# Kernel tuning notes

Measured on AMD Instinct MI355X. Metric: run time of the kernel, lower is better.

## Reference

```python
import jax, jax.numpy as jnp
import numpy as np

WIDTH = 1024
NH = 16
HD = 64
MBS = 16
B = 4
L = 2048
BASE_LR = 1.0
EPS = 1e-6


def gelu_tanh(x):
    return jax.nn.gelu(x, approximate=True)


def gelu_bwd(x):
    t = jnp.tanh(0.79788456 * x * (1 + 0.044715 * x * x))
    return 0.5 * x * ((1 - t * t) * (0.79788456 + 0.1070322243 * x * x)) + 0.5 * (1 + t)


def ln_fwd(x, g, b):
    mu = x.mean(-1, keepdims=True)
    var = ((x - mu) ** 2).mean(-1, keepdims=True)
    return g * ((x - mu) * jax.lax.rsqrt(var + EPS)) + b


def ln_l2_bwd(x, tgt, g, b):
    # grad of 0.5*||LN(x)-tgt||^2 wrt x
    mu = x.mean(-1, keepdims=True)
    var = ((x - mu) ** 2).mean(-1, keepdims=True)
    std = jnp.sqrt(var + EPS)
    xh = (x - mu) / std
    gx = (g * xh + b - tgt) * g
    return (gx - gx.mean(-1, keepdims=True) - xh * (gx * xh).mean(-1, keepdims=True)) / std


def adapter_forward(hidden_states, Wq, Wk, Wv, Wo, Wg, lr_w, lr_b,
                    learnable_token_idx, norm_w, norm_b, W1, b1, W2, b2,
                    post_w, post_b):
    Bb, Ll, width = hidden_states.shape
    nh, hd = norm_w.shape
    mbs = learnable_token_idx.shape[0]
    nc = Ll // mbs  # L chosen divisible by mini_batch_size

    def split_heads(x):  # [B,L,width] -> [B,nh,nc,mbs,hd]
        return x.reshape(Bb, Ll, nh, hd).transpose(0, 2, 1, 3).reshape(Bb, nh, nc, mbs, hd)

    XQ = split_heads(hidden_states @ Wq.T)
    XK = split_heads(hidden_states @ Wk.T)
    XV = split_heads(hidden_states @ Wv.T)

    # eta: learnable per-token lr gate (get_eta)
    X = hidden_states.reshape(Bb, nc, mbs, width)
    lr = jnp.einsum('bnkc,hdc->bhnkd', X, lr_w) + lr_b.reshape(1, nh, 1, 1, 1)
    lr = jax.nn.sigmoid(lr).transpose(0, 1, 2, 4, 3)  # [B,nh,nc,1,mbs]
    lr_eta = BASE_LR * lr / hd
    token_idx = jnp.clip(1.0 / jnp.arange(1, mbs + 1, dtype=hidden_states.dtype)
                         + learnable_token_idx, 0.0, None)
    token_eta = token_idx.reshape(1, 1, 1, mbs, 1)
    eta = token_eta * lr_eta  # [B,nh,nc,mbs,mbs]

    tril = jnp.tril(jnp.ones((mbs, mbs), dtype=hidden_states.dtype))
    lnw = norm_w.reshape(nh, 1, hd)
    lnb = norm_b.reshape(nh, 1, hd)

    def step(carry, xs):
        W1s, b1s, W2s, b2s = carry  # [B,nh,hd,4hd], [B,nh,1,4hd], [B,nh,4hd,hd], [B,nh,1,hd]
        XQm, XKm, XVm, etam = xs    # [B,nh,mbs,hd] x3, [B,nh,mbs,mbs]
        X1 = XKm
        Z1 = X1 @ W1s + b1s
        X2 = gelu_tanh(Z1)
        Z2 = X2 @ W2s + b2s
        gZ2 = ln_l2_bwd(Z2, XVm - XKm, lnw, lnb)
        gZ1 = (gZ2 @ jnp.swapaxes(W2s, -1, -2)) * gelu_bwd(Z1)
        eta_tril = etam * tril
        Attn1 = tril * (XQm @ jnp.swapaxes(X1, -1, -2))
        b1_bar = b1s - eta_tril @ gZ1
        Z1_bar = XQm @ W1s - (etam * Attn1) @ gZ1 + b1_bar
        X2_bar = gelu_tanh(Z1_bar)
        Attn2 = tril * (X2_bar @ jnp.swapaxes(X2, -1, -2))
        b2_bar = b2s - eta_tril @ gZ2
        Z2_bar = X2_bar @ W2s - (etam * Attn2) @ gZ2 + b2_bar
        last = etam[:, :, -1, :, None]  # [B,nh,mbs,1]
        W1n = W1s - jnp.swapaxes(last * X1, -1, -2) @ gZ1
        b1n = b1s - (last * gZ1).sum(-2, keepdims=True)
        W2n = W2s - jnp.swapaxes(last * X2, -1, -2) @ gZ2
        b2n = b2s - (last * gZ2).sum(-2, keepdims=True)
        XQW = XQm + ln_fwd(Z2_bar, lnw, lnb)
        return (W1n, b1n, W2n, b2n), XQW

    carry0 = (jnp.broadcast_to(W1, (Bb,) + W1.shape),
              jnp.broadcast_to(b1, (Bb,) + b1.shape),
              jnp.broadcast_to(W2, (Bb,) + W2.shape),
              jnp.broadcast_to(b2, (Bb,) + b2.shape))
    xs = tuple(jnp.moveaxis(t, 2, 0) for t in (XQ, XK, XV, eta))
    _, XQW = jax.lax.scan(step, carry0, xs)  # [nc,B,nh,mbs,hd]
    out = XQW.transpose(1, 0, 3, 2, 4).reshape(Bb, Ll, width)

    # post_norm (LayerNorm eps=1e-6)
    out = ln_fwd(out, post_w, post_b)
    # gate
    out = gelu_tanh(hidden_states @ Wg.T) * out
    # o_proj
    return out @ Wo.T


def setup_inputs():
    key = jax.random.key(0)
    ks = jax.random.split(key, 10)
    n = lambda k, s: jax.random.normal(k, s, dtype=jnp.float32) * 0.02
    return {
        'hidden_states': jax.random.normal(ks[0], (B, L, WIDTH), dtype=jnp.float32),
        'Wq': n(ks[1], (WIDTH, WIDTH)),
        'Wk': n(ks[2], (WIDTH, WIDTH)),
        'Wv': n(ks[3], (WIDTH, WIDTH)),
        'Wo': n(ks[4], (WIDTH, WIDTH)),
        'Wg': n(ks[5], (WIDTH, WIDTH)),
        'lr_w': n(ks[6], (NH, 1, WIDTH)),
        'lr_b': jnp.zeros((NH, 1), jnp.float32),
        'learnable_token_idx': jnp.zeros((MBS,), jnp.float32),
        'norm_w': jnp.ones((NH, HD), jnp.float32),
        'norm_b': jnp.zeros((NH, HD), jnp.float32),
        'W1': n(ks[7], (NH, HD, 4 * HD)),
        'b1': jnp.zeros((NH, 1, 4 * HD), jnp.float32),
        'W2': n(ks[8], (NH, 4 * HD, HD)),
        'b2': jnp.zeros((NH, 1, HD), jnp.float32),
        'post_w': jnp.ones((WIDTH,), jnp.float32),
        'post_b': jnp.zeros((WIDTH,), jnp.float32),
    }


def reference(hidden_states, Wq, Wk, Wv, Wo, Wg, lr_w, lr_b, learnable_token_idx,
              norm_w, norm_b, W1, b1, W2, b2, post_w, post_b):
    return adapter_forward(hidden_states, Wq, Wk, Wv, Wo, Wg, lr_w, lr_b,
                           learnable_token_idx, norm_w, norm_b, W1, b1, W2, b2,
                           post_w, post_b)
```

## Files before the change

kernel.cpp:

```cpp
#include <hip/hip_runtime.h>

#define WIDTH 1024
#define MBSZ 16
#define LLL 2048
#define NCHUNK 128

typedef __attribute__((ext_vector_type(4))) float f32x4;
typedef __attribute__((ext_vector_type(2))) float f32x2;
typedef __attribute__((ext_vector_type(8))) short short8;
typedef __attribute__((ext_vector_type(4))) short short4v;
typedef __attribute__((ext_vector_type(2))) unsigned u32x2;
typedef __attribute__((ext_vector_type(4))) unsigned u32x4;

#define MFMA16(a, b, c) __builtin_amdgcn_mfma_f32_16x16x32_bf16((a), (b), (c), 0, 0, 0)

__device__ __forceinline__ short f2bf(float f) {
  unsigned u = __float_as_uint(f);
  u = (u + 0x7FFFu + ((u >> 16) & 1u)) >> 16;
  return (short)u;
}
__device__ __forceinline__ float bf2f(short s) {
  return __uint_as_float(((unsigned)(unsigned short)s) << 16);
}
__device__ __forceinline__ unsigned cvt_pk(float lo, float hi) {
  unsigned r;
  asm("v_cvt_pk_bf16_f32 %0, %1, %2" : "=v"(r) : "v"(lo), "v"(hi));
  return r;
}
__device__ __forceinline__ float fast_e2u(float x) {
  return __builtin_amdgcn_exp2f(x * (2.30220776f + 0.10294322f * x * x));
}
__device__ __forceinline__ float gelu_f(float x) {
  float e = fast_e2u(x);
  return x * (1.0f - __builtin_amdgcn_rcpf(e + 1.0f));
}
__device__ __forceinline__ float gelu_bwd_f(float x) {
  float e = fast_e2u(x);
  float r = __builtin_amdgcn_rcpf(e + 1.0f);
  return 2.0f * x * r * (1.0f - r) * (0.79788456f + 0.1070322243f * x * x) + (1.0f - r);
}
__device__ __forceinline__ int w2row(int d) { return d * 264 + (d >> 3) * 24; }

template <int OUTBF>
__device__ __forceinline__ void gemm_64x128(const short* __restrict__ A,
                                            const short* __restrict__ W,
                                            float* __restrict__ C,
                                            short* __restrict__ Cb,
                                            int m0, int n0,
                                            short* sA, short* sB, int t2) {
  const int wv = t2 >> 6, ln = t2 & 63;
  const int fr = ln & 15, kh = (ln >> 4) * 8;
  const int arow = t2 >> 2, aseg = (t2 & 3) * 8;
  f32x4 acc[8];
#pragma unroll
  for (int s = 0; s < 8; ++s) acc[s] = (f32x4){0.f, 0.f, 0.f, 0.f};
  const short* ga = A + (long)(m0 + arow) * 1024 + aseg;
  const short* gw0 = W + (long)(n0 + arow) * 1024 + aseg;
  const short* gw1 = W + (long)(n0 + 64 + arow) * 1024 + aseg;
  for (int k0 = 0; k0 < 1024; k0 += 32) {
    const short8 a8 = *(const short8*)(ga + k0);
    const short8 w80 = *(const short8*)(gw0 + k0);
    const short8 w81 = *(const short8*)(gw1 + k0);
    *(short8*)&sA[arow * 40 + aseg] = a8;
    *(short8*)&sB[arow * 40 + aseg] = w80;
    *(short8*)&sB[(arow + 64) * 40 + aseg] = w81;
    __syncthreads();
    const short8 af = *(const short8*)&sA[(wv * 16 + fr) * 40 + kh];
#pragma unroll
    for (int s = 0; s < 8; ++s) {
      const short8 bf8 = *(const short8*)&sB[(s * 16 + fr) * 40 + kh];
      acc[s] = MFMA16(af, bf8, acc[s]);
    }
    __syncthreads();
  }
  const int orow = m0 + wv * 16 + (ln >> 4) * 4;
#pragma unroll
  for (int s = 0; s < 8; ++s)
#pragma unroll
    for (int q = 0; q < 4; ++q) {
      const long off = (long)(orow + q) * 1024 + n0 + s * 16 + fr;
      if (OUTBF) Cb[off] = f2bf(acc[s][q]);
      else C[off] = acc[s][q];
    }
}

__global__ __launch_bounds__(256) void cvt_kernel(const float* __restrict__ hs,
                                                  const float* __restrict__ Wq,
                                                  const float* __restrict__ Wk,
                                                  const float* __restrict__ Wv,
                                                  const float* __restrict__ Wg,
                                                  const float* __restrict__ Wo,
                                                  short* __restrict__ dst) {
  const long idx = ((long)blockIdx.x * 256 + threadIdx.x) * 8;
  if (idx >= 13631488L) return;
  const float* src;
  long off;
  if (idx < 8388608L)       { src = hs; off = idx; }
  else if (idx < 9437184L)  { src = Wq; off = idx - 8388608L; }
  else if (idx < 10485760L) { src = Wk; off = idx - 9437184L; }
  else if (idx < 11534336L) { src = Wv; off = idx - 10485760L; }
  else if (idx < 12582912L) { src = Wg; off = idx - 11534336L; }
  else                      { src = Wo; off = idx - 12582912L; }
  const f32x4 a = *(const f32x4*)(src + off);
  const f32x4 b = *(const f32x4*)(src + off + 4);
  u32x4 o;
  o[0] = cvt_pk(a[0], a[1]); o[1] = cvt_pk(a[2], a[3]);
  o[2] = cvt_pk(b[0], b[1]); o[3] = cvt_pk(b[2], b[3]);
  *(u32x4*)(dst + idx) = o;
}

__global__ __launch_bounds__(256) void gemm_final(const short* __restrict__ A,
                                                  const short* __restrict__ W,
                                                  float* __restrict__ C) {
  __shared__ __align__(16) short sA[2560];
  __shared__ __align__(16) short sB[5120];
  gemm_64x128<0>(A, W, C, nullptr, blockIdx.x * 64, blockIdx.y * 128, sA, sB, threadIdx.x);
}

__global__ __launch_bounds__(256) void qkv_lr_kernel(const short* __restrict__ hsb,
                                                     const short* __restrict__ Wqb,
                                                     const short* __restrict__ Wkb,
                                                     const short* __restrict__ Wvb,
                                                     float* __restrict__ Qb,
                                                     float* __restrict__ Kb,
                                                     float* __restrict__ Vb,
                                                     const float* __restrict__ hs,
                                                     const float* __restrict__ lrw,
                                                     const float* __restrict__ lrb,
                                                     float* __restrict__ LRb) {
  __shared__ __align__(16) short sA[2560];
  __shared__ __align__(16) short sB[5120];
  __shared__ __align__(16) float row[1024];
  const int tid = threadIdx.x;
  const int idx = blockIdx.x;
  if (idx < 3072) {
    const int which = idx >> 10, t = idx & 1023;
    const short* W = (which == 0) ? Wqb : (which == 1) ? Wkb : Wvb;
    float* C = (which == 0) ? Qb : (which == 1) ? Kb : Vb;
    gemm_64x128<0>(hsb, W, C, nullptr, (t & 127) * 64, (t >> 7) * 128, sA, sB, tid);
  } else {
    const int t = idx - 3072;
    *(f32x4*)&row[tid * 4] = *(const f32x4*)&hs[(long)t * 1024 + tid * 4];
    __syncthreads();
    const int hh = tid >> 4, j = tid & 15;
    const float* wrow = lrw + hh * 1024;
    float s = 0.f;
#pragma unroll 4
    for (int m = 0; m < 16; ++m) {
      const int c = j * 4 + m * 64;
      f32x4 x = *(const f32x4*)&row[c];
      f32x4 w = *(const f32x4*)&wrow[c];
      s += x[0] * w[0] + x[1] * w[1] + x[2] * w[2] + x[3] * w[3];
    }
#pragma unroll
    for (int o = 8; o; o >>= 1) s += __shfl_xor(s, o, 16);
    if (j == 0) {
      const float v = s + lrb[hh];
      const float sg = 1.f / (1.f + expf(-v));
      const int b = t >> 11, tr = t & 2047;
      LRb[((b << 4) + hh) * 2048 + tr] = sg * (1.f / 64.f);
    }
  }
}

__global__ __launch_bounds__(512, 2) void scan_gate_kernel(
    float* __restrict__ Qb, const float* __restrict__ Kb, const float* __restrict__ Vb,
    const float* __restrict__ LRb, const float* __restrict__ lti,
    const float* __restrict__ nw, const float* __restrict__ nb,
    const float* __restrict__ W1in, const float* __restrict__ b1in,
    const float* __restrict__ W2in, const float* __restrict__ b2in,
    const short* __restrict__ hsA, const short* __restrict__ Wgb,
    short* __restrict__ Gout) {
  __shared__ __align__(16) short sW1b[256 * 72];
  __shared__ __align__(16) short sW2dp[64 * 264 + 192];
  __shared__ __align__(16) short la1T[64 * 24];
  __shared__ __align__(16) short la2T[256 * 24];
  __shared__ __align__(16) short sX1b[16 * 72];
  __shared__ __align__(16) short sXQb[16 * 72];
  __shared__ __align__(16) float sXQf[16 * 68];
  __shared__ __align__(16) float sTg[16 * 72];
  __shared__ __align__(16) short sX2b[16 * 264];
  __shared__ __align__(16) short sXbb[16 * 264];
  __shared__ __align__(16) short sG1c[256 * 24];
  __shared__ __align__(16) short sG2b[16 * 72];
  __shared__ __align__(16) short sG2c[64 * 24];
  __shared__ __align__(16) float sZ2f[16 * 68];
  __shared__ __align__(16) short sC1b[16 * 24];
  __shared__ __align__(16) short sC2b[16 * 24];
  __shared__ __align__(16) float sB1[256];
  __shared__ __align__(16) float sB2[64];
  __shared__ float sLr[16];
  __shared__ float sTok[16];
  __shared__ __align__(16) float sLnw[64];
  __shared__ __align__(16) float sLnb[64];

  const int tid = threadIdx.x;

  if (blockIdx.x >= 64) {
    const int hh = tid >> 8, t2 = tid & 255;
    const int tile = (blockIdx.x - 64) * 2 + hh;
    short* sAh = sW1b + hh * 7680;
    short* sBh = sAh + 2560;
    gemm_64x128<1>(hsA, Wgb, nullptr, Gout, (tile & 127) * 64, (tile >> 7) * 128, sAh, sBh, t2);
    return;
  }

  const int bh = blockIdx.x, b = bh >> 4, h = bh & 15;
  const int w = tid >> 6, ln = tid & 63;
  const int fr = ln & 15, half = ln >> 4, hk = half * 8;
  const int nt0 = 2 * w;

  float w1m[8][4], w2m[8][4];
#pragma unroll
  for (int r = 0; r < 8; ++r) {
    const int T = w * 8 + r, dt = T >> 4, pt = T & 15;
#pragma unroll
    for (int qq = 0; qq < 4; ++qq) {
      w1m[r][qq] = W1in[h * 16384 + (dt * 16 + half * 4 + qq) * 256 + pt * 16 + fr];
      w2m[r][qq] = W2in[h * 16384 + (pt * 16 + half * 4 + qq) * 64 + dt * 16 + fr];
    }
  }
  for (int e = tid; e < 16384; e += 512) {
    {
      const int d = e >> 8, p = e & 255;
      sW1b[p * 72 + d] = f2bf(W1in[h * 16384 + e]);
    }
    {
      const int p = e >> 6, d = e & 63;
      sW2dp[w2row(d) + (p ^ (((d >> 3) & 3) << 3))] = f2bf(W2in[h * 16384 + e]);
    }
  }
  if (tid < 256) sB1[tid] = b1in[h * 256 + tid];
  if (tid < 64) { sB2[tid] = b2in[h * 64 + tid]; sLnw[tid] = nw[h * 64 + tid]; sLnb[tid] = nb[h * 64 + tid]; }
  if (tid < 16) sTok[tid] = fmaxf(1.0f / (float)(tid + 1) + lti[tid], 0.0f);

  const f32x4 zf4 = (f32x4){0.f, 0.f, 0.f, 0.f};
  short8 zs8;
#pragma unroll
  for (int j = 0; j < 8; ++j) zs8[j] = 0;

  const int pf_i = tid >> 5;
  const int pf_d = (tid & 31) * 2;
  f32x2 pk, pq, pv;
  float plr = 0.f;
  {
    const long a0 = ((long)(b * LLL + pf_i)) * WIDTH + h * 64 + pf_d;
    pk = *(const f32x2*)&Kb[a0];
    pq = *(const f32x2*)&Qb[a0];
    pv = *(const f32x2*)&Vb[a0];
    if (tid < 16) plr = LRb[(long)bh * 2048 + tid];
  }

  for (int n = 0; n < NCHUNK; ++n) {
    const long gbase = ((long)(b * LLL + n * MBSZ)) * WIDTH + h * 64;

    {
      *(unsigned*)&sX1b[pf_i * 72 + pf_d] = cvt_pk(pk[0], pk[1]);
      *(unsigned*)&sXQb[pf_i * 72 + pf_d] = cvt_pk(pq[0], pq[1]);
      sXQf[pf_i * 68 + pf_d] = pq[0];
      sXQf[pf_i * 68 + pf_d + 1] = pq[1];
      sTg[pf_i * 72 + pf_d] = pv[0] - pk[0];
      sTg[pf_i * 72 + pf_d + 1] = pv[1] - pk[1];
      if (tid < 16) sLr[tid] = plr;
    }
    __syncthreads();

    short8 aX1[2], aXQ[2];
    aX1[0] = *(const short8*)&sX1b[fr * 72 + hk];
    aX1[1] = *(const short8*)&sX1b[fr * 72 + 32 + hk];
    aXQ[0] = *(const short8*)&sXQb[fr * 72 + hk];
    aXQ[1] = *(const short8*)&sXQb[fr * 72 + 32 + hk];
    f32x4 z1[2], q1[2];
    float b1p[2];
#pragma unroll
    for (int t = 0; t < 2; ++t) {
      const int p = (nt0 + t) * 16 + fr;
      z1[t] = zf4; q1[t] = zf4;
#pragma unroll
      for (int ks = 0; ks < 2; ++ks) {
        short8 bw = *(const short8*)&sW1b[p * 72 + ks * 32 + hk];
        z1[t] = MFMA16(aX1[ks], bw, z1[t]);
        q1[t] = MFMA16(aXQ[ks], bw, q1[t]);
      }
      b1p[t] = sB1[p];
#pragma unroll
      for (int qq = 0; qq < 4; ++qq) {
        z1[t][qq] += b1p[t];
        sX2b[(half * 4 + qq) * 264 + p] = f2bf(gelu_f(z1[t][qq]));
      }
    }
    {
      const float tok15 = sTok[15];
      const int d = tid >> 3, j0 = (tid & 7) * 2;
      const float v0 = bf2f(sX1b[j0 * 72 + d]) * (tok15 * sLr[j0]);
      const float v1 = bf2f(sX1b[(j0 + 1) * 72 + d]) * (tok15 * sLr[j0 + 1]);
      *(unsigned*)&la1T[d * 24 + j0] = cvt_pk(v0, v1);
    }
    if (w == 0) {
      f32x4 c = MFMA16(aXQ[0], aX1[0], zf4);
      c = MFMA16(aXQ[1], aX1[1], c);
#pragma unroll
      for (int qq = 0; qq < 4; ++qq) {
        const int i = half * 4 + qq, j = fr;
        sC1b[i * 24 + j] = f2bf((i >= j) ? sTok[i] * sLr[j] * (c[qq] + 1.0f) : 0.0f);
      }
    }
    __syncthreads();

    float bb2old = 0.f;
    if (w < 4) {
      const int d = w * 16 + fr;
      const int sw = ((d >> 3) & 3) << 3;
      const int rb = w2row(d);
      f32x4 za = zf4, zb = zf4;
#pragma unroll
      for (int ks = 0; ks < 4; ++ks) {
        short8 a = *(const short8*)&sX2b[fr * 264 + ks * 32 + hk];
        short8 bfr = *(const short8*)&sW2dp[rb + ((ks * 32 + hk) ^ sw)];
        za = MFMA16(a, bfr, za);
      }
#pragma unroll
      for (int ks = 4; ks < 8; ++ks) {
        short8 a = *(const short8*)&sX2b[fr * 264 + ks * 32 + hk];
        short8 bfr = *(const short8*)&sW2dp[rb + ((ks * 32 + hk) ^ sw)];
        zb = MFMA16(a, bfr, zb);
      }
      bb2old = sB2[d];
#pragma unroll
      for (int qq = 0; qq < 4; ++qq)
        sZ2f[(half * 4 + qq) * 68 + d] = za[qq] + zb[qq] + bb2old;
    }
    __syncthreads();

    if (tid < 256) {
      const int i = tid >> 4, j4 = tid & 15;
      const f32x4 z = *(const f32x4*)&sZ2f[i * 68 + j4 * 4];
      float s1 = z[0] + z[1] + z[2] + z[3];
      float s2 = z[0] * z[0] + z[1] * z[1] + z[2] * z[2] + z[3] * z[3];
#pragma unroll
      for (int o = 8; o; o >>= 1) { s1 += __shfl_xor(s1, o, 16); s2 += __shfl_xor(s2, o, 16); }
      const float mu = s1 * (1.f / 64.f);
      const float rstd = rsqrtf(s2 * (1.f / 64.f) - mu * mu + 1e-6f);
      const f32x4 g = *(const f32x4*)&sLnw[j4 * 4];
      const f32x4 bb = *(const f32x4*)&sLnb[j4 * 4];
      const f32x4 tg = *(const f32x4*)&sTg[i * 72 + j4 * 4];
      f32x4 xh, gx;
      float a1 = 0.f, a2 = 0.f;
#pragma unroll
      for (int e = 0; e < 4; ++e) {
        xh[e] = (z[e] - mu) * rstd;
        gx[e] = (g[e] * xh[e] + bb[e] - tg[e]) * g[e];
        a1 += gx[e]; a2 += gx[e] * xh[e];
      }
#pragma unroll
      for (int o = 8; o; o >>= 1) { a1 += __shfl_xor(a1, o, 16); a2 += __shfl_xor(a2, o, 16); }
      const float m1 = a1 * (1.f / 64.f), m2 = a2 * (1.f / 64.f);
      float o4[4];
#pragma unroll
      for (int e = 0; e < 4; ++e) o4[e] = (gx[e] - m1 - xh[e] * m2) * rstd;
      const unsigned lo = cvt_pk(o4[0], o4[1]);
      const unsigned hi = cvt_pk(o4[2], o4[3]);
      *(u32x2*)&sG2b[i * 72 + j4 * 4] = (u32x2){lo, hi};
      sG2c[(j4 * 4 + 0) * 24 + i] = (short)lo;
      sG2c[(j4 * 4 + 1) * 24 + i] = (short)(lo >> 16);
      sG2c[(j4 * 4 + 2) * 24 + i] = (short)hi;
      sG2c[(j4 * 4 + 3) * 24 + i] = (short)(hi >> 16);
    } else {
      const int pp = tid - 256;
      const float tok15 = sTok[15];
      unsigned uu[8];
#pragma unroll
      for (int jp = 0; jp < 8; ++jp) {
        const float v0 = bf2f(sX2b[(2 * jp) * 264 + pp]) * (tok15 * sLr[2 * jp]);
        const float v1 = bf2f(sX2b[(2 * jp + 1) * 264 + pp]) * (tok15 * sLr[2 * jp + 1]);
        uu[jp] = cvt_pk(v0, v1);
      }
      *(u32x4*)&la2T[pp * 24] = (u32x4){uu[0], uu[1], uu[2], uu[3]};
      *(u32x4*)&la2T[pp * 24 + 8] = (u32x4){uu[4], uu[5], uu[6], uu[7]};
    }
    __syncthreads();

    {
      short8 aG2[2];
      aG2[0] = *(const short8*)&sG2b[fr * 72 + hk];
      aG2[1] = *(const short8*)&sG2b[fr * 72 + 32 + hk];
#pragma unroll
      for (int t = 0; t < 2; ++t) {
        const int p = (nt0 + t) * 16 + fr;
        f32x4 g = zf4;
#pragma unroll
        for (int ks = 0; ks < 2; ++ks) {
          const int dg = ks * 32 + hk;
          const int rb2 = w2row(dg) + (p ^ (((dg >> 3) & 3) << 3));
          short8 bw;
#pragma unroll
          for (int jj = 0; jj < 8; ++jj) bw[jj] = sW2dp[rb2 + jj * 264];
          g = MFMA16(aG2[ks], bw, g);
        }
        const unsigned lo = cvt_pk(g[0] * gelu_bwd_f(z1[t][0]), g[1] * gelu_bwd_f(z1[t][1]));
        const unsigned hi = cvt_pk(g[2] * gelu_bwd_f(z1[t][2]), g[3] * gelu_bwd_f(z1[t][3]));
        *(u32x2*)&sG1c[p * 24 + half * 4] = (u32x2){lo, hi};
      }
    }
    if (tid < 64) {
      float s = 0.f;
#pragma unroll
      for (int k = 0; k < 4; ++k) {
        const short4v g4 = *(const short4v*)&sG2c[tid * 24 + k * 4];
        const f32x4 lr4 = *(const f32x4*)&sLr[k * 4];
        s += lr4[0] * bf2f(g4[0]) + lr4[1] * bf2f(g4[1]) +
             lr4[2] * bf2f(g4[2]) + lr4[3] * bf2f(g4[3]);
      }
      sB2[tid] -= sTok[15] * s;
    }
    __syncthreads();

    {
      short8 ac = zs8;
      if (half < 2) ac = *(const short8*)&sC1b[fr * 24 + hk];
#pragma unroll
      for (int t = 0; t < 2; ++t) {
        const int p = (nt0 + t) * 16 + fr;
        short8 bg = zs8;
        if (half < 2) bg = *(const short8*)&sG1c[p * 24 + hk];
        f32x4 corr = MFMA16(ac, bg, zf4);
#pragma unroll
        for (int qq = 0; qq < 4; ++qq)
          sXbb[(half * 4 + qq) * 264 + p] = f2bf(gelu_f(q1[t][qq] + b1p[t] - corr[qq]));
      }
    }
    {
#pragma unroll
      for (int r = 0; r < 8; ++r) {
        const int T = w * 8 + r, dt = T >> 4, pt = T & 15;
        short8 af = zs8, bg = zs8;
        if (half < 2) {
          af = *(const short8*)&la1T[(dt * 16 + fr) * 24 + hk];
          bg = *(const short8*)&sG1c[(pt * 16 + fr) * 24 + hk];
        }
        f32x4 dl = MFMA16(af, bg, zf4);
        const int pp = pt * 16 + fr, d0 = dt * 16 + half * 4;
        w1m[r][0] -= dl[0]; w1m[r][1] -= dl[1]; w1m[r][2] -= dl[2]; w1m[r][3] -= dl[3];
        const unsigned lo = cvt_pk(w1m[r][0], w1m[r][1]);
        const unsigned hi = cvt_pk(w1m[r][2], w1m[r][3]);
        *(u32x2*)&sW1b[pp * 72 + d0] = (u32x2){lo, hi};
      }
    }
    if (tid < 256) {
      float s = 0.f;
#pragma unroll
      for (int k = 0; k < 4; ++k) {
        const short4v g4 = *(const short4v*)&sG1c[tid * 24 + k * 4];
        const f32x4 lr4 = *(const f32x4*)&sLr[k * 4];
        s += lr4[0] * bf2f(g4[0]) + lr4[1] * bf2f(g4[1]) +
             lr4[2] * bf2f(g4[2]) + lr4[3] * bf2f(g4[3]);
      }
      sB1[tid] -= sTok[15] * s;
    }
    __syncthreads();

    {
      const int nn = (n + 1 < NCHUNK) ? n + 1 : n;
      const long a1 = ((long)(b * LLL + nn * MBSZ + pf_i)) * WIDTH + h * 64 + pf_d;
      pk = *(const f32x2*)&Kb[a1];
      pq = *(const f32x2*)&Qb[a1];
      pv = *(const f32x2*)&Vb[a1];
      if (tid < 16) plr = LRb[(long)bh * 2048 + nn * MBSZ + tid];
    }
    f32x4 zbar = zf4;
    if (w < 4) {
      const int d = w * 16 + fr;
      const int sw = ((d >> 3) & 3) << 3;
      const int rb = w2row(d);
      f32x4 za = zf4, zb = zf4;
#pragma unroll
      for (int ks = 0; ks < 4; ++ks) {
        short8 a = *(const short8*)&sXbb[fr * 264 + ks * 32 + hk];
        short8 bfr = *(const short8*)&sW2dp[rb + ((ks * 32 + hk) ^ sw)];
        za = MFMA16(a, bfr, za);
      }
#pragma unroll
      for (int ks = 4; ks < 8; ++ks) {
        short8 a = *(const short8*)&sXbb[fr * 264 + ks * 32 + hk];
        short8 bfr = *(const short8*)&sW2dp[rb + ((ks * 32 + hk) ^ sw)];
        zb = MFMA16(a, bfr, zb);
      }
      zbar[0] = za[0] + zb[0]; zbar[1] = za[1] + zb[1];
      zbar[2] = za[2] + zb[2]; zbar[3] = za[3] + zb[3];
    } else if (w == 4) {
      f32x4 c = zf4;
#pragma unroll
      for (int ks = 0; ks < 8; ++ks) {
        short8 a = *(const short8*)&sXbb[fr * 264 + ks * 32 + hk];
        short8 bx = *(const short8*)&sX2b[fr * 264 + ks * 32 + hk];
        c = MFMA16(a, bx, c);
      }
#pragma unroll
      for (int qq = 0; qq < 4; ++qq) {
        const int i = half * 4 + qq, j = fr;
        sC2b[i * 24 + j] = f2bf((i >= j) ? sTok[i] * sLr[j] * (c[qq] + 1.0f) : 0.0f);
      }
    }
    __syncthreads();

    if (w < 4) {
      const int d = w * 16 + fr;
      short8 ac = zs8, bg = zs8;
      if (half < 2) {
        ac = *(const short8*)&sC2b[fr * 24 + hk];
        bg = *(const short8*)&sG2c[d * 24 + hk];
      }
      f32x4 corr = MFMA16(ac, bg, zf4);
#pragma unroll
      for (int qq = 0; qq < 4; ++qq)
        sZ2f[(half * 4 + qq) * 68 + d] = zbar[qq] + bb2old - corr[qq];
    }
    {
#pragma unroll
      for (int r = 0; r < 8; ++r) {
        const int T = w * 8 + r, pt = T & 15, dt = T >> 4;
        short8 af = zs8, bg = zs8;
        if (half < 2) {
          af = *(const short8*)&la2T[(pt * 16 + fr) * 24 + hk];
          bg = *(const short8*)&sG2c[(dt * 16 + fr) * 24 + hk];
        }
        f32x4 dl = MFMA16(af, bg, zf4);
        const int dd = dt * 16 + fr;
        const int swp = ((dd >> 3) & 3) << 3;
        const int p0 = pt * 16 + half * 4;
        w2m[r][0] -= dl[0]; w2m[r][1] -= dl[1]; w2m[r][2] -= dl[2]; w2m[r][3] -= dl[3];
        const unsigned lo = cvt_pk(w2m[r][0], w2m[r][1]);
        const unsigned hi = cvt_pk(w2m[r][2], w2m[r][3]);
        *(u32x2*)&sW2dp[w2row(dd) + (p0 ^ swp)] = (u32x2){lo, hi};
      }
    }
    __syncthreads();

    if (tid < 256) {
      const int i = tid >> 4, j4 = tid & 15;
      const f32x4 z = *(const f32x4*)&sZ2f[i * 68 + j4 * 4];
      float s1 = z[0] + z[1] + z[2] + z[3];
      float s2 = z[0] * z[0] + z[1] * z[1] + z[2] * z[2] + z[3] * z[3];
#pragma unroll
      for (int o = 8; o; o >>= 1) { s1 += __shfl_xor(s1, o, 16); s2 += __shfl_xor(s2, o, 16); }
      const float mu = s1 * (1.f / 64.f);
      const float rstd = rsqrtf(s2 * (1.f / 64.f) - mu * mu + 1e-6f);
      const f32x4 g = *(const f32x4*)&sLnw[j4 * 4];
      const f32x4 bb = *(const f32x4*)&sLnb[j4 * 4];
      const f32x4 xq = *(const f32x4*)&sXQf[i * 68 + j4 * 4];
      f32x4 o4;
#pragma unroll
      for (int e = 0; e < 4; ++e) o4[e] = xq[e] + g[e] * ((z[e] - mu) * rstd) + bb[e];
      *(f32x4*)&Qb[gbase + (long)i * WIDTH + j4 * 4] = o4;
    }
    __syncthreads();
  }
}

__global__ __launch_bounds__(256) void epi_kernel(const float* __restrict__ X,
                                                  const short* __restrict__ G,
                                                  const float* __restrict__ pw,
                                                  const float* __restrict__ pb,
                                                  short* __restrict__ T) {
  __shared__ float red[8];
  const int t = blockIdx.x, tid = threadIdx.x;
  const long base = (long)t * 1024 + tid * 4;
  f32x4 x = *(const f32x4*)&X[base];
  float s1 = x[0] + x[1] + x[2] + x[3];
  float s2 = x[0] * x[0] + x[1] * x[1] + x[2] * x[2] + x[3] * x[3];
#pragma unroll
  for (int o = 32; o; o >>= 1) { s1 += __shfl_xor(s1, o, 64); s2 += __shfl_xor(s2, o, 64); }
  const int wv = tid >> 6, ln = tid & 63;
  if (ln == 0) { red[wv] = s1; red[4 + wv] = s2; }
  __syncthreads();
  s1 = red[0] + red[1] + red[2] + red[3];
  s2 = red[4] + red[5] + red[6] + red[7];
  const float mu = s1 * (1.f / 1024.f);
  const float rstd = rsqrtf(s2 * (1.f / 1024.f) - mu * mu + 1e-6f);
  const short4v g4 = *(const short4v*)&G[base];
  f32x4 w = *(const f32x4*)&pw[tid * 4];
  f32x4 bb = *(const f32x4*)&pb[tid * 4];
  float o4[4];
#pragma unroll
  for (int e = 0; e < 4; ++e) {
    float y = w[e] * ((x[e] - mu) * rstd) + bb[e];
    o4[e] = gelu_f(bf2f(g4[e])) * y;
  }
  *(u32x2*)&T[base] = (u32x2){cvt_pk(o4[0], o4[1]), cvt_pk(o4[2], o4[3])};
}

extern "C" void kernel_launch(void* const* d_in, const int* in_sizes, int n_in,
                              void* d_out, int out_size, void* d_ws, size_t ws_size,
                              hipStream_t stream) {
  const float* hs  = (const float*)d_in[0];
  const float* Wq  = (const float*)d_in[1];
  const float* Wk  = (const float*)d_in[2];
  const float* Wv  = (const float*)d_in[3];
  const float* Wo  = (const float*)d_in[4];
  const float* Wg  = (const float*)d_in[5];
  const float* lrw = (const float*)d_in[6];
  const float* lrb = (const float*)d_in[7];
  const float* lti = (const float*)d_in[8];
  const float* nw  = (const float*)d_in[9];
  const float* nb  = (const float*)d_in[10];
  const float* W1  = (const float*)d_in[11];
  const float* b1  = (const float*)d_in[12];
  const float* W2  = (const float*)d_in[13];
  const float* b2  = (const float*)d_in[14];
  const float* pw  = (const float*)d_in[15];
  const float* pb  = (const float*)d_in[16];
  float* out = (float*)d_out;
  float* ws = (float*)d_ws;

  float* Qb  = ws;
  float* Kb  = ws + 8388608;
  float* Vb  = ws + 16777216;
  float* LRb = ws + 25165824;
  short* hsb = (short*)(ws + 25296896);
  short* Wqb = hsb + 8388608;
  short* Wkb = Wqb + 1048576;
  short* Wvb = Wkb + 1048576;
  short* Wgb = Wvb + 1048576;
  short* Wob = Wgb + 1048576;
  short* Tb  = (short*)Kb;
  short* Gbb = (short*)out;

  cvt_kernel<<<6656, 256, 0, stream>>>(hs, Wq, Wk, Wv, Wg, Wo, hsb);
  qkv_lr_kernel<<<11264, 256, 0, stream>>>(hsb, Wqb, Wkb, Wvb, Qb, Kb, Vb, hs, lrw, lrb, LRb);
  scan_gate_kernel<<<576, 512, 0, stream>>>(Qb, Kb, Vb, LRb, lti, nw, nb, W1, b1, W2, b2,
                                            hsb, Wgb, Gbb);
  epi_kernel<<<8192, 256, 0, stream>>>(Qb, Gbb, pw, pb, Tb);
  gemm_final<<<dim3(128, 8), 256, 0, stream>>>(Tb, Wob, out);
}
```

Baseline: 918.1 us.

## Double-buffer chunk inputs in LDS and merge barrier phases in scan loop

Chunk inputs (K, Q, V-K target and lr gate) now go into double-buffered shared arrays. Idle threads 256-511 write the next chunk's data during the final LayerNorm/output phase instead of in a separate phase with its own barrier at the top of the loop. The b2 update is moved into the same phase as the corrected-activation computation, which removes another __syncthreads per chunk. Prefetch loads are widened to float4 on half the threads. The cost is more LDS and fewer threads doing the prefetch.

Result: no change. 928.7 us (+1.1%).

```diff
diff --git a/kernel.cpp b/kernel.cpp
--- a/kernel.cpp
+++ b/kernel.cpp
@@ -175,10 +175,10 @@
   __shared__ __align__(16) short sW2dp[64 * 264 + 192];
   __shared__ __align__(16) short la1T[64 * 24];
   __shared__ __align__(16) short la2T[256 * 24];
-  __shared__ __align__(16) short sX1b[16 * 72];
-  __shared__ __align__(16) short sXQb[16 * 72];
-  __shared__ __align__(16) float sXQf[16 * 68];
-  __shared__ __align__(16) float sTg[16 * 72];
+  __shared__ __align__(16) short sX1b[2][16 * 72];
+  __shared__ __align__(16) short sXQb[2][16 * 72];
+  __shared__ __align__(16) float sXQf[2][16 * 68];
+  __shared__ __align__(16) float sTg[2][16 * 72];
   __shared__ __align__(16) short sX2b[16 * 264];
   __shared__ __align__(16) short sXbb[16 * 264];
   __shared__ __align__(16) short sG1c[256 * 24];
@@ -189,7 +189,7 @@
   __shared__ __align__(16) short sC2b[16 * 24];
   __shared__ __align__(16) float sB1[256];
   __shared__ __align__(16) float sB2[64];
-  __shared__ float sLr[16];
+  __shared__ float sLr2[2][16];
   __shared__ float sTok[16];
   __shared__ __align__(16) float sLnw[64];
   __shared__ __align__(16) float sLnb[64];
@@ -239,37 +239,37 @@
 #pragma unroll
   for (int j = 0; j < 8; ++j) zs8[j] = 0;
 
-  const int pf_i = tid >> 5;
-  const int pf_d = (tid & 31) * 2;
-  f32x2 pk, pq, pv;
+  const int ct = tid - 256;
+  const int ci = ct >> 4;
+  const int cd = (ct & 15) * 4;
+  f32x4 pk4, pq4, pv4;
   float plr = 0.f;
-  {
-    const long a0 = ((long)(b * LLL + pf_i)) * WIDTH + h * 64 + pf_d;
-    pk = *(const f32x2*)&Kb[a0];
-    pq = *(const f32x2*)&Qb[a0];
-    pv = *(const f32x2*)&Vb[a0];
-    if (tid < 16) plr = LRb[(long)bh * 2048 + tid];
-  }
+  if (tid >= 256) {
+    const long a0 = ((long)(b * LLL + ci)) * WIDTH + h * 64 + cd;
+    pk4 = *(const f32x4*)&Kb[a0];
+    pq4 = *(const f32x4*)&Qb[a0];
+    pv4 = *(const f32x4*)&Vb[a0];
+    if (ct < 16) plr = LRb[(long)bh * 2048 + ct];
+    *(u32x2*)&sX1b[0][ci * 72 + cd] = (u32x2){cvt_pk(pk4[0], pk4[1]), cvt_pk(pk4[2], pk4[3])};
+    *(u32x2*)&sXQb[0][ci * 72 + cd] = (u32x2){cvt_pk(pq4[0], pq4[1]), cvt_pk(pq4[2], pq4[3])};
+    *(f32x4*)&sXQf[0][ci * 68 + cd] = pq4;
+    f32x4 tg4;
+#pragma unroll
+    for (int e = 0; e < 4; ++e) tg4[e] = pv4[e] - pk4[e];
+    *(f32x4*)&sTg[0][ci * 72 + cd] = tg4;
+    if (ct < 16) sLr2[0][ct] = plr;
+  }
+  __syncthreads();
 
   for (int n = 0; n < NCHUNK; ++n) {
+    const int cb = n & 1;
     const long gbase = ((long)(b * LLL + n * MBSZ)) * WIDTH + h * 64;
 
-    {
-      *(unsigned*)&sX1b[pf_i * 72 + pf_d] = cvt_pk(pk[0], pk[1]);
-      *(unsigned*)&sXQb[pf_i * 72 + pf_d] = cvt_pk(pq[0], pq[1]);
-      sXQf[pf_i * 68 + pf_d] = pq[0];
-      sXQf[pf_i * 68 + pf_d + 1] = pq[1];
-      sTg[pf_i * 72 + pf_d] = pv[0] - pk[0];
-      sTg[pf_i * 72 + pf_d + 1] = pv[1] - pk[1];
-      if (tid < 16) sLr[tid] = plr;
-    }
-    __syncthreads();
-
     short8 aX1[2], aXQ[2];
-    aX1[0] = *(const short8*)&sX1b[fr * 72 + hk];
-    aX1[1] = *(const short8*)&sX1b[fr * 72 + 32 + hk];
-    aXQ[0] = *(const short8*)&sXQb[fr * 72 + hk];
-    aXQ[1] = *(const short8*)&sXQb[fr * 72 + 32 + hk];
+    aX1[0] = *(const short8*)&sX1b[cb][fr * 72 + hk];
+    aX1[1] = *(const short8*)&sX1b[cb][fr * 72 + 32 + hk];
+    aXQ[0] = *(const short8*)&sXQb[cb][fr * 72 + hk];
+    aXQ[1] = *(const short8*)&sXQb[cb][fr * 72 + 32 + hk];
     f32x4 z1[2], q1[2];
     float b1p[2];
 #pragma unroll
@@ -292,8 +292,8 @@
     {
       const float tok15 = sTok[15];
       const int d = tid >> 3, j0 = (tid & 7) * 2;
-      const float v0 = bf2f(sX1b[j0 * 72 + d]) * (tok15 * sLr[j0]);
-      const float v1 = bf2f(sX1b[(j0 + 1) * 72 + d]) * (tok15 * sLr[j0 + 1]);
+      const float v0 = bf2f(sX1b[cb][j0 * 72 + d]) * (tok15 * sLr2[cb][j0]);
+      const float v1 = bf2f(sX1b[cb][(j0 + 1) * 72 + d]) * (tok15 * sLr2[cb][j0 + 1]);
       *(unsigned*)&la1T[d * 24 + j0] = cvt_pk(v0, v1);
     }
     if (w == 0) {
@@ -302,7 +302,7 @@
 #pragma unroll
       for (int qq = 0; qq < 4; ++qq) {
         const int i = half * 4 + qq, j = fr;
-        sC1b[i * 24 + j] = f2bf((i >= j) ? sTok[i] * sLr[j] * (c[qq] + 1.0f) : 0.0f);
+        sC1b[i * 24 + j] = f2bf((i >= j) ? sTok[i] * sLr2[cb][j] * (c[qq] + 1.0f) : 0.0f);
       }
     }
     __syncthreads();
@@ -343,7 +343,7 @@
       const float rstd = rsqrtf(s2 * (1.f / 64.f) - mu * mu + 1e-6f);
       const f32x4 g = *(const f32x4*)&sLnw[j4 * 4];
       const f32x4 bb = *(const f32x4*)&sLnb[j4 * 4];
-      const f32x4 tg = *(const f32x4*)&sTg[i * 72 + j4 * 4];
+      const f32x4 tg = *(const f32x4*)&sTg[cb][i * 72 + j4 * 4];
       f32x4 xh, gx;
       float a1 = 0.f, a2 = 0.f;
 #pragma unroll
@@ -371,8 +371,8 @@
       unsigned uu[8];
 #pragma unroll
       for (int jp = 0; jp < 8; ++jp) {
-        const float v0 = bf2f(sX2b[(2 * jp) * 264 + pp]) * (tok15 * sLr[2 * jp]);
-        const float v1 = bf2f(sX2b[(2 * jp + 1) * 264 + pp]) * (tok15 * sLr[2 * jp + 1]);
+        const float v0 = bf2f(sX2b[(2 * jp) * 264 + pp]) * (tok15 * sLr2[cb][2 * jp]);
+        const float v1 = bf2f(sX2b[(2 * jp + 1) * 264 + pp]) * (tok15 * sLr2[cb][2 * jp + 1]);
         uu[jp] = cvt_pk(v0, v1);
       }
       *(u32x4*)&la2T[pp * 24] = (u32x4){uu[0], uu[1], uu[2], uu[3]};
@@ -402,19 +402,6 @@
         *(u32x2*)&sG1c[p * 24 + half * 4] = (u32x2){lo, hi};
       }
     }
-    if (tid < 64) {
-      float s = 0.f;
-#pragma unroll
-      for (int k = 0; k < 4; ++k) {
-        const short4v g4 = *(const short4v*)&sG2c[tid * 24 + k * 4];
-        const f32x4 lr4 = *(const f32x4*)&sLr[k * 4];
-        s += lr4[0] * bf2f(g4[0]) + lr4[1] * bf2f(g4[1]) +
-             lr4[2] * bf2f(g4[2]) + lr4[3] * bf2f(g4[3]);
-      }
-      sB2[tid] -= sTok[15] * s;
-    }
-    __syncthreads();
-
     {
       short8 ac = zs8;
       if (half < 2) ac = *(const short8*)&sC1b[fr * 24 + hk];
@@ -429,6 +416,19 @@
           sXbb[(half * 4 + qq) * 264 + p] = f2bf(gelu_f(q1[t][qq] + b1p[t] - corr[qq]));
       }
     }
+    if (tid < 64) {
+      float s = 0.f;
+#pragma unroll
+      for (int k = 0; k < 4; ++k) {
+        const short4v g4 = *(const short4v*)&sG2c[tid * 24 + k * 4];
+        const f32x4 lr4 = *(const f32x4*)&sLr2[cb][k * 4];
+        s += lr4[0] * bf2f(g4[0]) + lr4[1] * bf2f(g4[1]) +
+             lr4[2] * bf2f(g4[2]) + lr4[3] * bf2f(g4[3]);
+      }
+      sB2[tid] -= sTok[15] * s;
+    }
+    __syncthreads();
+
     {
 #pragma unroll
       for (int r = 0; r < 8; ++r) {
@@ -451,7 +451,7 @@
 #pragma unroll
       for (int k = 0; k < 4; ++k) {
         const short4v g4 = *(const short4v*)&sG1c[tid * 24 + k * 4];
-        const f32x4 lr4 = *(const f32x4*)&sLr[k * 4];
+        const f32x4 lr4 = *(const f32x4*)&sLr2[cb][k * 4];
         s += lr4[0] * bf2f(g4[0]) + lr4[1] * bf2f(g4[1]) +
              lr4[2] * bf2f(g4[2]) + lr4[3] * bf2f(g4[3]);
       }
@@ -459,13 +459,13 @@
     }
     __syncthreads();
 
-    {
+    if (tid >= 256) {
       const int nn = (n + 1 < NCHUNK) ? n + 1 : n;
-      const long a1 = ((long)(b * LLL + nn * MBSZ + pf_i)) * WIDTH + h * 64 + pf_d;
-      pk = *(const f32x2*)&Kb[a1];
-      pq = *(const f32x2*)&Qb[a1];
-      pv = *(const f32x2*)&Vb[a1];
-      if (tid < 16) plr = LRb[(long)bh * 2048 + nn * MBSZ + tid];
+      const long a1 = ((long)(b * LLL + nn * MBSZ + ci)) * WIDTH + h * 64 + cd;
+      pk4 = *(const f32x4*)&Kb[a1];
+      pq4 = *(const f32x4*)&Qb[a1];
+      pv4 = *(const f32x4*)&Vb[a1];
+      if (ct < 16) plr = LRb[(long)bh * 2048 + nn * MBSZ + ct];
     }
     f32x4 zbar = zf4;
     if (w < 4) {
@@ -498,7 +498,7 @@
 #pragma unroll
       for (int qq = 0; qq < 4; ++qq) {
         const int i = half * 4 + qq, j = fr;
-        sC2b[i * 24 + j] = f2bf((i >= j) ? sTok[i] * sLr[j] * (c[qq] + 1.0f) : 0.0f);
+        sC2b[i * 24 + j] = f2bf((i >= j) ? sTok[i] * sLr2[cb][j] * (c[qq] + 1.0f) : 0.0f);
       }
     }
     __syncthreads();
@@ -547,11 +547,21 @@
       const float rstd = rsqrtf(s2 * (1.f / 64.f) - mu * mu + 1e-6f);
       const f32x4 g = *(const f32x4*)&sLnw[j4 * 4];
       const f32x4 bb = *(const f32x4*)&sLnb[j4 * 4];
-      const f32x4 xq = *(const f32x4*)&sXQf[i * 68 + j4 * 4];
+      const f32x4 xq = *(const f32x4*)&sXQf[cb][i * 68 + j4 * 4];
       f32x4 o4;
 #pragma unroll
       for (int e = 0; e < 4; ++e) o4[e] = xq[e] + g[e] * ((z[e] - mu) * rstd) + bb[e];
       *(f32x4*)&Qb[gbase + (long)i * WIDTH + j4 * 4] = o4;
+    } else {
+      const int nb2 = cb ^ 1;
+      *(u32x2*)&sX1b[nb2][ci * 72 + cd] = (u32x2){cvt_pk(pk4[0], pk4[1]), cvt_pk(pk4[2], pk4[3])};
+      *(u32x2*)&sXQb[nb2][ci * 72 + cd] = (u32x2){cvt_pk(pq4[0], pq4[1]), cvt_pk(pq4[2], pq4[3])};
+      *(f32x4*)&sXQf[nb2][ci * 68 + cd] = pq4;
+      f32x4 tg4;
+#pragma unroll
+      for (int e = 0; e < 4; ++e) tg4[e] = pv4[e] - pk4[e];
+      *(f32x4*)&sTg[nb2][ci * 72 + cd] = tg4;
+      if (ct < 16) sLr2[nb2][ct] = plr;
     }
     __syncthreads();
   }
```
